# Performance work log

Hardware: AMD Instinct MI355X
Metric: run time of the kernel (lower is better)

Reference implementation:

```python
import jax, jax.numpy as jnp
import numpy as np

B, CIN, H, W = 2, 128, 64, 64
CHNN = 32
SC = 100.0


def conv1x1(x, w, b=None):
    # x: (b,c,h,w), w: (o,c)
    y = jnp.einsum('bchw,oc->bohw', x, w)
    return y if b is None else y + b[None, :, None, None]


def depthwise5x5_replicate(x, w, b):
    # x: (b,c,h,w), w: (c,1,5,5), replicate (edge) padding of 2
    xp = jnp.pad(x, ((0, 0), (0, 0), (2, 2), (2, 2)), mode='edge')
    y = jax.lax.conv_general_dilated(xp, w, (1, 1), 'VALID',
                                     feature_group_count=x.shape[1])
    return y + b[None, :, None, None]


def grid_sample_bilinear(img, grid):
    # img: (b,C,Hs,Ws); grid: (b,h,w,2) with (x,y) in [-1,1]; align_corners=True
    b, C, Hs, Ws = img.shape
    x = (grid[..., 0] + 1.0) * 0.5 * (Ws - 1)
    y = (grid[..., 1] + 1.0) * 0.5 * (Hs - 1)
    x0 = jnp.floor(x); y0 = jnp.floor(y)
    wx1 = x - x0; wx0 = 1.0 - wx1
    wy1 = y - y0; wy0 = 1.0 - wy1
    x0i = jnp.clip(x0, 0, Ws - 1).astype(jnp.int32)
    x1i = jnp.clip(x0 + 1, 0, Ws - 1).astype(jnp.int32)
    y0i = jnp.clip(y0, 0, Hs - 1).astype(jnp.int32)
    y1i = jnp.clip(y0 + 1, 0, Hs - 1).astype(jnp.int32)
    imgf = img.reshape(b, C, Hs * Ws)

    def gather(idx):  # idx: (b,h,w) int32 -> (b,C,h,w)
        idxf = idx.reshape(b, -1)
        out = jax.vmap(lambda im, ix: im[:, ix])(imgf, idxf)
        return out.reshape(b, C, idx.shape[1], idx.shape[2])

    v00 = gather(y0i * Ws + x0i)
    v01 = gather(y0i * Ws + x1i)
    v10 = gather(y1i * Ws + x0i)
    v11 = gather(y1i * Ws + x1i)
    return (v00 * (wy0 * wx0)[:, None] + v01 * (wy0 * wx1)[:, None]
            + v10 * (wy1 * wx0)[:, None] + v11 * (wy1 * wx1)[:, None])


def setup_inputs() -> dict:
    key = jax.random.key(0)
    ks = jax.random.split(key, 8)
    return {
        'feat': jax.random.normal(ks[0], (B, CIN, H, W), jnp.float32),
        'gauss': jax.random.uniform(ks[1], (B, H, W, H, W), jnp.float32),
        'W_in': jax.random.normal(ks[2], (CHNN, 1), jnp.float32) * 0.1,
        'b_in': jnp.zeros((CHNN,), jnp.float32),
        'W_dw': jax.random.normal(ks[3], (CHNN, 1, 5, 5), jnp.float32) * 0.1,
        'b_dw': jnp.zeros((CHNN,), jnp.float32),
        'W_ofs': jax.random.normal(ks[4], (2, CHNN), jnp.float32) * 0.1,
        'W_a': jax.random.normal(ks[5], (1, CHNN), jnp.float32) * 0.1,
        'b_a': jnp.zeros((1,), jnp.float32),
        'lam': jnp.full((1,), 0.1, jnp.float32),
    }


def reference(feat, gauss, W_in, b_in, W_dw, b_dw, W_ofs, W_a, b_a, lam):
    b, _, h, w = feat.shape
    fm = feat.mean(1, keepdims=True)                       # (b,1,h,w)
    feat_in = conv1x1(fm, W_in, b_in)                      # (b,chnn,h,w)
    z = jax.nn.relu(depthwise5x5_replicate(feat_in, W_dw, b_dw))
    ofs = jnp.tanh(conv1x1(z, W_ofs))                      # (b,2,h,w)
    scale = jnp.array([1.0 / h, 1.0 / w], dtype=feat.dtype).reshape(1, 2, 1, 1)
    ofs = jnp.transpose(ofs * scale, (0, 2, 3, 1))         # (b,h,w,2) as (y,x)
    yy = (jnp.linspace(0.5, h - 0.5, h, dtype=feat.dtype) / h) * 2.0 - 1.0
    xx = (jnp.linspace(0.5, w - 0.5, w, dtype=feat.dtype) / w) * 2.0 - 1.0
    ref = jnp.stack(jnp.meshgrid(yy, xx, indexing='ij'), -1)  # (h,w,2)
    pos = jnp.clip(SC * ofs + ref[None], -1.0, 1.0)
    grid = pos[..., ::-1]                                  # (x,y) order
    # gauss (b,u,v,h,w) -> rearrange to (b,h,w,u,v) -> flatten (h,w) as channels
    g = jnp.transpose(gauss, (0, 3, 4, 1, 2)).reshape(b, h * w, h, w)
    gd = grid_sample_bilinear(g, grid).reshape(b, h, w, h, w)
    feat_a = conv1x1(feat_in, W_a, b_a)                    # (b,1,h,w)
    ga = 1.0 + lam[0] * feat_a                             # (b,1,h,w)
    return gd * ga[:, :, None, :, :]
```

## Files before the change

kernel.cpp:

```cpp
#include <hip/hip_runtime.h>
#include <math.h>

#define HW 64
#define NB 2
#define NCIN 128
#define NCH 32

typedef float f32x4 __attribute__((ext_vector_type(4)));


__global__ __launch_bounds__(256) void k_mean(const float* __restrict__ feat,
                                              float* __restrict__ fm) {
    int bh = blockIdx.x;
    int w  = threadIdx.x & 63;
    int cg = threadIdx.x >> 6;
    int b = bh >> 6, h = bh & 63;
    const float* base = feat + ((size_t)(b * NCIN) * 64 + h) * 64 + w;
    float s = 0.f;
    #pragma unroll
    for (int c = 0; c < 32; ++c)
        s += base[(size_t)(cg * 32 + c) * 4096];
    __shared__ float red[4][64];
    red[cg][w] = s;
    __syncthreads();
    if (cg == 0) {
        float tot = red[0][w] + red[1][w] + red[2][w] + red[3][w];
        fm[bh * 64 + w] = tot * (1.f / 128.f);
    }
}

__global__ __launch_bounds__(256) void k_params(
    const float* __restrict__ fm,
    const float* __restrict__ W_in, const float* __restrict__ b_in,
    const float* __restrict__ W_dw, const float* __restrict__ b_dw,
    const float* __restrict__ W_ofs, const float* __restrict__ W_a,
    const float* __restrict__ b_a, const float* __restrict__ lam,
    int4* __restrict__ offs, float4* __restrict__ wts)
{
    __shared__ float WD[NCH * 25];
    __shared__ float Wi[NCH], Bi[NCH], Bd[NCH], Wo0[NCH], Wo1[NCH], Wa_s[NCH];
    int t = threadIdx.x;
    for (int k = t; k < NCH * 25; k += 256) WD[k] = W_dw[k];
    if (t < NCH) {
        Wi[t]  = W_in[t];  Bi[t]  = b_in[t]; Bd[t] = b_dw[t];
        Wo0[t] = W_ofs[t]; Wo1[t] = W_ofs[NCH + t];
        Wa_s[t] = W_a[t];
    }
    __syncthreads();

    int p = blockIdx.x * 256 + t;
    int b = p >> 12;
    int i = (p >> 6) & 63;
    int j = p & 63;

    float patch[25];
    #pragma unroll
    for (int dy = 0; dy < 5; ++dy) {
        int ry = i + dy - 2; ry = ry < 0 ? 0 : (ry > 63 ? 63 : ry);
        #pragma unroll
        for (int dx = 0; dx < 5; ++dx) {
            int rx = j + dx - 2; rx = rx < 0 ? 0 : (rx > 63 ? 63 : rx);
            patch[dy * 5 + dx] = fm[(b * 64 + ry) * 64 + rx];
        }
    }
    float fmc = patch[12];

    float a0 = 0.f, a1 = 0.f, kA = 0.f, kB = 0.f;
    for (int c = 0; c < NCH; ++c) {
        float s = 0.f, sw = 0.f;
        #pragma unroll
        for (int q = 0; q < 25; ++q) {
            float wv = WD[c * 25 + q];
            s  += patch[q] * wv;
            sw += wv;
        }
        float pre = Wi[c] * s + Bi[c] * sw + Bd[c];
        float zc = pre > 0.f ? pre : 0.f;
        a0 += zc * Wo0[c];
        a1 += zc * Wo1[c];
        kA += Wi[c] * Wa_s[c];
        kB += Bi[c] * Wa_s[c];
    }
    float ga = 1.f + lam[0] * (fmc * kA + kB + b_a[0]);

    float yy = (i + 0.5f) * (1.f / 32.f) - 1.f;
    float xx = (j + 0.5f) * (1.f / 32.f) - 1.f;
    float pos0 = fminf(fmaxf((100.f / 64.f) * tanhf(a0) + yy, -1.f), 1.f);
    float pos1 = fminf(fmaxf((100.f / 64.f) * tanhf(a1) + xx, -1.f), 1.f);
    float y = (pos0 + 1.f) * 0.5f * 63.f;
    float x = (pos1 + 1.f) * 0.5f * 63.f;
    float y0 = floorf(y), x0 = floorf(x);
    float wy1 = y - y0, wx1 = x - x0;
    float wy0 = 1.f - wy1, wx0 = 1.f - wx1;
    int y0i = (int)y0; y0i = y0i < 0 ? 0 : (y0i > 63 ? 63 : y0i);
    int x0i = (int)x0; x0i = x0i < 0 ? 0 : (x0i > 63 ? 63 : x0i);
    int y1i = y0i + 1 > 63 ? 63 : y0i + 1;
    int x1i = x0i + 1 > 63 ? 63 : x0i + 1;

    int basep = b * 16777216;
    offs[p] = make_int4(basep + (y0i * 64 + x0i) * 4096,
                        basep + (y0i * 64 + x1i) * 4096,
                        basep + (y1i * 64 + x0i) * 4096,
                        basep + (y1i * 64 + x1i) * 4096);
    wts[p] = make_float4(wy0 * wx0 * ga, wy0 * wx1 * ga,
                         wy1 * wx0 * ga, wy1 * wx1 * ga);
}

__global__ __launch_bounds__(256) void k_sample(
    const float* __restrict__ gauss,
    const int4* __restrict__ offs, const float4* __restrict__ wts,
    float* __restrict__ out)
{
    __shared__ float lds[128 * 64];
    int bid = blockIdx.x;
    int swz = (bid & 7) * 512 + (bid >> 3);
    int ct = swz & 31;
    int bi = swz >> 5;
    int b = bi >> 6, i = bi & 63;
    int c0 = ct * 128;
    int t  = threadIdx.x;
    int pbase = bi * 64;

    int h  = t & 31;
    int js = t >> 5;

    #pragma unroll
    for (int r = 0; r < 8; ++r) {
        int j = r * 8 + js;
        int4  off = offs[pbase + j];
        float4 wt = wts[pbase + j];
        f32x4 A = *((const f32x4*)(gauss + off.x + c0) + h);
        f32x4 B = *((const f32x4*)(gauss + off.y + c0) + h);
        f32x4 C = *((const f32x4*)(gauss + off.z + c0) + h);
        f32x4 D = *((const f32x4*)(gauss + off.w + c0) + h);
        f32x4 res = wt.x * A + wt.y * B + wt.z * C + wt.w * D;
        *(f32x4*)&lds[j * 128 + 4 * (h ^ (j & 7))] = res;
    }
    __syncthreads();

    size_t obase = (size_t)b * 16777216 + (size_t)c0 * 4096 + (size_t)i * 64;
    int j   = t & 63;
    int cq0 = t >> 6;
    #pragma unroll
    for (int m = 0; m < 8; ++m) {
        int cquad = m * 4 + cq0;
        f32x4 v = *(const f32x4*)&lds[j * 128 + 4 * (cquad ^ (j & 7))];
        float* po = out + obase + (size_t)(4 * cquad) * 4096 + j;
        __builtin_nontemporal_store(v.x, po);
        __builtin_nontemporal_store(v.y, po + 4096);
        __builtin_nontemporal_store(v.z, po + 8192);
        __builtin_nontemporal_store(v.w, po + 12288);
    }
}

extern "C" void kernel_launch(void* const* d_in, const int* in_sizes, int n_in,
                              void* d_out, int out_size, void* d_ws, size_t ws_size,
                              hipStream_t stream) {
    const float* feat  = (const float*)d_in[0];
    const float* gauss = (const float*)d_in[1];
    const float* W_in  = (const float*)d_in[2];
    const float* b_in  = (const float*)d_in[3];
    const float* W_dw  = (const float*)d_in[4];
    const float* b_dw  = (const float*)d_in[5];
    const float* W_ofs = (const float*)d_in[6];
    const float* W_a   = (const float*)d_in[7];
    const float* b_a   = (const float*)d_in[8];
    const float* lam   = (const float*)d_in[9];
    float* out = (float*)d_out;

    float* fm   = (float*)d_ws;
    int4*  offs = (int4*)((char*)d_ws + 32768);
    float4* wts = (float4*)((char*)d_ws + 32768 + 131072);

    k_mean  <<<NB * HW, 256, 0, stream>>>(feat, fm);
    k_params<<<32, 256, 0, stream>>>(fm, W_in, b_in, W_dw, b_dw,
                                     W_ofs, W_a, b_a, lam, offs, wts);
    k_sample<<<NB * HW * 32, 256, 0, stream>>>(gauss, offs, wts, out);
}
```

Baseline: 61.64 us.

## Load gauss corners directly to LDS and blend during transpose-store

Measured after the change: 112.7 us. 1.83x slower.

```diff
diff --git a/kernel.cpp b/kernel.cpp
--- a/kernel.cpp
+++ b/kernel.cpp
@@ -7,6 +7,12 @@
 #define NCH 32
 
 typedef float f32x4 __attribute__((ext_vector_type(4)));
+
+typedef __attribute__((address_space(3))) void lds_void;
+typedef const __attribute__((address_space(1))) void g_void;
+__device__ __forceinline__ void load_lds16(const float* g, float* l) {
+    __builtin_amdgcn_global_load_lds((g_void*)g, (lds_void*)l, 16, 0, 0);
+}
 
 
 __global__ __launch_bounds__(256) void k_mean(const float* __restrict__ feat,
@@ -111,45 +117,55 @@
     const int4* __restrict__ offs, const float4* __restrict__ wts,
     float* __restrict__ out)
 {
-    __shared__ float lds[128 * 64];
+    __shared__ float ldsbuf[32 * 256];
     int bid = blockIdx.x;
-    int swz = (bid & 7) * 512 + (bid >> 3);
-    int ct = swz & 31;
-    int bi = swz >> 5;
+    int swz = (bid & 7) * 2048 + (bid >> 3);
+    int bi  = swz >> 7;
+    int mid = swz & 127;
+    int ct  = mid >> 1;
+    int jh  = mid & 1;
     int b = bi >> 6, i = bi & 63;
-    int c0 = ct * 128;
+    int c0 = ct * 64;
     int t  = threadIdx.x;
-    int pbase = bi * 64;
+    int pbase = bi * 64 + jh * 32;
 
-    int h  = t & 31;
-    int js = t >> 5;
-
+    int w    = t >> 6;
+    int lane = t & 63;
+    int m    = lane & 15;
+    int c2   = lane >> 4;
     #pragma unroll
     for (int r = 0; r < 8; ++r) {
-        int j = r * 8 + js;
-        int4  off = offs[pbase + j];
-        float4 wt = wts[pbase + j];
-        f32x4 A = *((const f32x4*)(gauss + off.x + c0) + h);
-        f32x4 B = *((const f32x4*)(gauss + off.y + c0) + h);
-        f32x4 C = *((const f32x4*)(gauss + off.z + c0) + h);
-        f32x4 D = *((const f32x4*)(gauss + off.w + c0) + h);
-        f32x4 res = wt.x * A + wt.y * B + wt.z * C + wt.w * D;
-        *(f32x4*)&lds[j * 128 + 4 * (h ^ (j & 7))] = res;
+        int j2 = w * 8 + r;
+        int4 o = offs[pbase + j2];
+        int offsel = c2 < 2 ? (c2 == 0 ? o.x : o.y)
+                            : (c2 == 2 ? o.z : o.w);
+        const float* gp = gauss + (size_t)(offsel + c0)
+                        + ((m ^ (j2 & 15)) << 2);
+        load_lds16(gp, &ldsbuf[j2 * 256]);
     }
     __syncthreads();
 
-    size_t obase = (size_t)b * 16777216 + (size_t)c0 * 4096 + (size_t)i * 64;
-    int j   = t & 63;
-    int cq0 = t >> 6;
+    int j2 = t & 31;
+    int cg = t >> 5;
+    float4 wt = wts[pbase + j2];
+    size_t obase = (size_t)b * 16777216 + (size_t)c0 * 4096
+                 + (size_t)i * 64 + jh * 32 + j2;
+    int sbase = j2 * 256;
+    int f = j2 & 15;
     #pragma unroll
-    for (int m = 0; m < 8; ++m) {
-        int cquad = m * 4 + cq0;
-        f32x4 v = *(const f32x4*)&lds[j * 128 + 4 * (cquad ^ (j & 7))];
-        float* po = out + obase + (size_t)(4 * cquad) * 4096 + j;
-        __builtin_nontemporal_store(v.x, po);
-        __builtin_nontemporal_store(v.y, po + 4096);
-        __builtin_nontemporal_store(v.z, po + 8192);
-        __builtin_nontemporal_store(v.w, po + 12288);
+    for (int u = 0; u < 2; ++u) {
+        int q = cg * 2 + u;
+        int pos = (q ^ f) * 4;
+        f32x4 A = *(const f32x4*)&ldsbuf[sbase +       pos];
+        f32x4 B = *(const f32x4*)&ldsbuf[sbase +  64 + pos];
+        f32x4 C = *(const f32x4*)&ldsbuf[sbase + 128 + pos];
+        f32x4 D = *(const f32x4*)&ldsbuf[sbase + 192 + pos];
+        f32x4 res = wt.x * A + wt.y * B + wt.z * C + wt.w * D;
+        float* po = out + obase + (size_t)(q * 4) * 4096;
+        __builtin_nontemporal_store(res.x, po);
+        __builtin_nontemporal_store(res.y, po + 4096);
+        __builtin_nontemporal_store(res.z, po + 8192);
+        __builtin_nontemporal_store(res.w, po + 12288);
     }
 }
 
@@ -175,5 +191,5 @@
     k_mean  <<<NB * HW, 256, 0, stream>>>(feat, fm);
     k_params<<<32, 256, 0, stream>>>(fm, W_in, b_in, W_dw, b_dw,
                                      W_ofs, W_a, b_a, lam, offs, wts);
-    k_sample<<<NB * HW * 32, 256, 0, stream>>>(gauss, offs, wts, out);
+    k_sample<<<NB * HW * 128, 256, 0, stream>>>(gauss, offs, wts, out);
 }
```
